# Kernel tuning notes

Measured on AMD Instinct MI355X. Metric: run time of the kernel, lower is better.

## Reference

```python
import jax, jax.numpy as jnp
import numpy as np

L = 16
IN0 = 7  # 3 + 3 + 1 per the torch module
CH = [16, 32, 16]
N = 500000
NEG_SLOPE = 0.2


def setup_inputs() -> dict:
    key = jax.random.key(0)
    ks = jax.random.split(key, 5)
    x = jax.random.normal(ks[0], (N, IN0), dtype=jnp.float32)
    idx = jax.random.randint(ks[1], (N,), 0, L, dtype=jnp.int32)
    # kaiming-uniform-like init scale per layer fan-in
    def init_w(k, shape):
        fan_in = shape[1]
        bound = float(np.sqrt(6.0 / fan_in))
        return jax.random.uniform(k, shape, dtype=jnp.float32, minval=-bound, maxval=bound)
    W0 = init_w(ks[2], (L, IN0, CH[0]))
    W1 = init_w(ks[3], (L, CH[0], CH[1]))
    W2 = init_w(ks[4], (L, CH[1], CH[2]))
    b0 = jnp.zeros((L, CH[0]), dtype=jnp.float32)
    b1 = jnp.zeros((L, CH[1]), dtype=jnp.float32)
    b2 = jnp.zeros((L, CH[2]), dtype=jnp.float32)
    return {"x": x, "idx": idx, "W0": W0, "b0": b0, "W1": W1, "b1": b1, "W2": W2, "b2": b2}


def reference(x, idx, W0, b0, W1, b1, W2, b2):
    # Per-point expert-indexed MLP: h <- LeakyReLU(h @ W[idx] + b[idx]) per layer.
    h = x
    for W, b in ((W0, b0), (W1, b1), (W2, b2)):
        # gather per-point weight [N, in, out] and bias [N, out], vec-mat per point
        h = jax.nn.leaky_relu(
            jnp.einsum("nc,nco->no", h, W[idx]) + b[idx],
            negative_slope=NEG_SLOPE,
        )
    return h
```

## Files before the change

kernel.cpp:

```cpp
#include <hip/hip_runtime.h>
#include <hip/hip_fp16.h>


#define L_EXP 16
#define IN0   7
#define C0    16
#define C1    32
#define C2    16
#define NEG   0.2f
#define BLK   256
#define MPT   4
#define SEGPAD (BLK * MPT)
#define CHUNK  1024
#define NBM    512

#define NW0T 2048
#define NW1T 8192
#define NW2T 8192
#define NWT_TOT (NW0T + NW1T + NW2T)
#define PREPBLK (NWT_TOT / BLK)

#define WS_PART  64
#define WB_W0T   33792
#define WB_W1T   37888
#define WB_W2T   54272
#define WS_PERM  18432

typedef _Float16 h2 __attribute__((ext_vector_type(2)));
union F4H { float4 f4; h2 h[4]; };

__device__ __forceinline__ h2 pk(float a, float b) {
    return __builtin_bit_cast(h2, __builtin_amdgcn_cvt_pkrtz(a, b));
}

__global__ void k_hist(const int* __restrict__ idx, int n, int nblk,
                       int* __restrict__ ws,
                       const float* __restrict__ W0,
                       const float* __restrict__ W1,
                       const float* __restrict__ W2) {
    int t = threadIdx.x;
    if (blockIdx.x >= nblk) {
        int k = (blockIdx.x - nblk) * BLK + t;
        __half* hW0 = (__half*)((char*)ws + WB_W0T);
        __half* hW1 = (__half*)((char*)ws + WB_W1T);
        __half* hW2 = (__half*)((char*)ws + WB_W2T);
        if (k < NW0T) {
            int e = k >> 7, r = k & 127, o = r >> 3, c = r & 7;
            float v = (c < IN0) ? W0[e * (IN0 * C0) + c * C0 + o] : 0.0f;
            hW0[k] = __float2half(v);
        } else if (k < NW0T + NW1T) {
            int k2 = k - NW0T;
            int e = k2 >> 9, r = k2 & 511, o = r >> 4, c = r & 15;
            hW1[k2] = __float2half(W1[e * (C0 * C1) + c * C1 + o]);
        } else {
            int k2 = k - NW0T - NW1T;
            int e = k2 >> 9, r = k2 & 511, o = r >> 5, c = r & 31;
            hW2[k2] = __float2half(W2[e * (C1 * C2) + c * C2 + o]);
        }
        return;
    }
    __shared__ int bins[L_EXP];
    if (t < L_EXP) bins[t] = 0;
    __syncthreads();
    int i4 = blockIdx.x * CHUNK + t * 4;
    if (i4 + 3 < n) {
        int4 v = *reinterpret_cast<const int4*>(idx + i4);
        atomicAdd(&bins[v.x & 15], 1);
        atomicAdd(&bins[v.y & 15], 1);
        atomicAdd(&bins[v.z & 15], 1);
        atomicAdd(&bins[v.w & 15], 1);
    } else {
#pragma unroll
        for (int q = 0; q < 4; ++q)
            if (i4 + q < n) atomicAdd(&bins[idx[i4 + q] & 15], 1);
    }
    __syncthreads();
    if (t < L_EXP) ws[WS_PART + t * NBM + blockIdx.x] = bins[t];
}

__global__ void k_scan(int* __restrict__ ws, int nblk) {
    int t = threadIdx.x;
    int e = t >> 6, l = t & 63;
    int running = 0;
    for (int c = 0; c < nblk; c += 64) {
        int b = c + l;
        int v = (b < nblk) ? ws[WS_PART + e * NBM + b] : 0;
        int s = v;
#pragma unroll
        for (int d = 1; d < 64; d <<= 1) {
            int u = __shfl_up(s, d, 64);
            if (l >= d) s += u;
        }
        if (b < nblk) ws[WS_PART + e * NBM + b] = running + (s - v);
        running += __shfl(s, 63, 64);
    }
    if (l == 0) ws[e] = running;
    __syncthreads();
    if (t == 0) {
        int run = 0;
        for (int q = 0; q < L_EXP; ++q) {
            ws[16 + q] = run;
            run += ((ws[q] + SEGPAD - 1) / SEGPAD) * SEGPAD;
        }
        ws[32] = run;
    }
}

__global__ void k_scatter(const int* __restrict__ idx, int n,
                          int* __restrict__ ws) {
    __shared__ int soff[L_EXP];
    __shared__ int lcount[L_EXP];
    int t = threadIdx.x;
    if (t < L_EXP) {
        soff[t] = ws[16 + t] + ws[WS_PART + t * NBM + blockIdx.x];
        lcount[t] = 0;
    }
    __syncthreads();
    int i4 = blockIdx.x * CHUNK + t * 4;
#pragma unroll
    for (int q = 0; q < 4; ++q) {
        int i = i4 + q;
        if (i < n) {
            int e = idx[i] & 15;
            int r = atomicAdd(&lcount[e], 1);
            ws[WS_PERM + soff[e] + r] = i;
        }
    }
}

__device__ __forceinline__ float leaky(float a) { return fmaxf(a, NEG * a); }

__device__ __forceinline__ float fdot2(h2 a, h2 b, float c) {
    return __builtin_amdgcn_fdot2(a, b, c, false);
}

__global__ void __launch_bounds__(BLK, 2) k_mlp(
    const int* __restrict__ meta, const float* __restrict__ x,
    const float* __restrict__ b0, const float* __restrict__ b1,
    const float* __restrict__ b2, float* __restrict__ out) {
    __shared__ __align__(16) __half sW0t[C0 * 8];
    __shared__ __align__(16) __half sW1t[C1 * C0];
    __shared__ __align__(16) __half sW2t[C2 * C1];
    __shared__ __align__(16) float sB0[C0];
    __shared__ __align__(16) float sB1[C1];
    __shared__ __align__(16) float sB2[C2];

    int start = blockIdx.x * SEGPAD;
    if (start >= meta[32]) return;

    int e = 0;
    while (start >= meta[16 + e + 1]) ++e;
    e = __builtin_amdgcn_readfirstlane(e);

    int t = threadIdx.x;
    {
        const int* w0i = (const int*)((const char*)meta + WB_W0T) + e * 64;
        const int* w1i = (const int*)((const char*)meta + WB_W1T) + e * 256;
        const int* w2i = (const int*)((const char*)meta + WB_W2T) + e * 256;
        if (t < 64) reinterpret_cast<int*>(sW0t)[t] = w0i[t];
        reinterpret_cast<int*>(sW1t)[t] = w1i[t];
        reinterpret_cast<int*>(sW2t)[t] = w2i[t];
        if (t >= 128 && t < 128 + C0) sB0[t - 128] = b0[e * C0 + (t - 128)];
        if (t >= 160 && t < 160 + C1) sB1[t - 160] = b1[e * C1 + (t - 160)];
        if (t >= 192 && t < 192 + C2) sB2[t - 192] = b2[e * C2 + (t - 192)];
    }
    __syncthreads();

    int seg = meta[16 + e];
    int cnt = meta[e];
    int j0 = start - seg + t;

    h2  xh[MPT][4];
    int pid[MPT];
    bool act[MPT];
#pragma unroll
    for (int m = 0; m < MPT; ++m) {
        int j = j0 + m * BLK;
        act[m] = (j < cnt);
        int p = meta[WS_PERM + seg + j];
        pid[m] = act[m] ? p : 0;
        const float* xp = x + (size_t)pid[m] * IN0;
        float4 a = *reinterpret_cast<const float4*>(xp);
        float4 b = *reinterpret_cast<const float4*>(xp + 3);
        xh[m][0] = pk(a.x, a.y);
        xh[m][1] = pk(a.z, a.w);
        xh[m][2] = pk(b.y, b.z);
        xh[m][3] = pk(b.w, 0.0f);
    }
    __builtin_amdgcn_sched_barrier(0);

    float h0f[MPT][C0];
#pragma unroll
    for (int o = 0; o < C0; ++o) {
        F4H u;
        u.f4 = *reinterpret_cast<const float4*>(&sW0t[o * 8]);
#pragma unroll
        for (int m = 0; m < MPT; ++m) {
            float a = sB0[o];
            a = fdot2(xh[m][0], u.h[0], a);
            a = fdot2(xh[m][1], u.h[1], a);
            a = fdot2(xh[m][2], u.h[2], a);
            a = fdot2(xh[m][3], u.h[3], a);
            h0f[m][o] = leaky(a);
        }
        if (o == 7) __builtin_amdgcn_sched_barrier(0);
    }
    h2 h0h[MPT][8];
#pragma unroll
    for (int m = 0; m < MPT; ++m)
#pragma unroll
        for (int p = 0; p < 8; ++p)
            h0h[m][p] = pk(h0f[m][2 * p], h0f[m][2 * p + 1]);
    __builtin_amdgcn_sched_barrier(0);

    float h2a[MPT][C2];
#pragma unroll
    for (int m = 0; m < MPT; ++m)
#pragma unroll
        for (int o = 0; o < C2; ++o) h2a[m][o] = sB2[o];
#pragma unroll 1
    for (int ch = 0; ch < C1 / 8; ++ch) {
        float tvf[MPT][8];
#pragma unroll
        for (int o8 = 0; o8 < 8; ++o8) {
            int o = ch * 8 + o8;
            F4H ua, ub;
            ua.f4 = reinterpret_cast<const float4*>(&sW1t[o * C0])[0];
            ub.f4 = reinterpret_cast<const float4*>(&sW1t[o * C0])[1];
#pragma unroll
            for (int m = 0; m < MPT; ++m) {
                float a = sB1[o];
                a = fdot2(h0h[m][0], ua.h[0], a);
                a = fdot2(h0h[m][1], ua.h[1], a);
                a = fdot2(h0h[m][2], ua.h[2], a);
                a = fdot2(h0h[m][3], ua.h[3], a);
                a = fdot2(h0h[m][4], ub.h[0], a);
                a = fdot2(h0h[m][5], ub.h[1], a);
                a = fdot2(h0h[m][6], ub.h[2], a);
                a = fdot2(h0h[m][7], ub.h[3], a);
                tvf[m][o8] = leaky(a);
            }
        }
        __builtin_amdgcn_sched_barrier(0);
        h2 tvh[MPT][4];
#pragma unroll
        for (int m = 0; m < MPT; ++m)
#pragma unroll
            for (int p = 0; p < 4; ++p)
                tvh[m][p] = pk(tvf[m][2 * p], tvf[m][2 * p + 1]);
#pragma unroll
        for (int o = 0; o < C2; ++o) {
            F4H u;
            u.f4 = *reinterpret_cast<const float4*>(&sW2t[o * C1 + ch * 8]);
#pragma unroll
            for (int m = 0; m < MPT; ++m) {
                float a = h2a[m][o];
                a = fdot2(tvh[m][0], u.h[0], a);
                a = fdot2(tvh[m][1], u.h[1], a);
                a = fdot2(tvh[m][2], u.h[2], a);
                a = fdot2(tvh[m][3], u.h[3], a);
                h2a[m][o] = a;
            }
        }
        __builtin_amdgcn_sched_barrier(0);
    }

#pragma unroll
    for (int m = 0; m < MPT; ++m) {
        if (act[m]) {
            float4* outp = reinterpret_cast<float4*>(out + (size_t)pid[m] * C2);
#pragma unroll
            for (int og = 0; og < C2 / 4; ++og) {
                float4 o;
                o.x = leaky(h2a[m][og * 4 + 0]);
                o.y = leaky(h2a[m][og * 4 + 1]);
                o.z = leaky(h2a[m][og * 4 + 2]);
                o.w = leaky(h2a[m][og * 4 + 3]);
                outp[og] = o;
            }
        }
    }
}

extern "C" void kernel_launch(void* const* d_in, const int* in_sizes, int n_in,
                              void* d_out, int out_size, void* d_ws, size_t ws_size,
                              hipStream_t stream) {
    const float* x  = (const float*)d_in[0];
    const int*  idx = (const int*)d_in[1];
    const float* W0 = (const float*)d_in[2];
    const float* b0 = (const float*)d_in[3];
    const float* W1 = (const float*)d_in[4];
    const float* b1 = (const float*)d_in[5];
    const float* W2 = (const float*)d_in[6];
    const float* b2 = (const float*)d_in[7];
    float* out = (float*)d_out;

    int n = in_sizes[1];
    int* ws = (int*)d_ws;

    int nblk = (n + CHUNK - 1) / CHUNK;
    k_hist<<<nblk + PREPBLK, BLK, 0, stream>>>(idx, n, nblk, ws, W0, W1, W2);
    k_scan<<<1, 1024, 0, stream>>>(ws, nblk);
    k_scatter<<<nblk, BLK, 0, stream>>>(idx, n, ws);

    int mblk = (n + L_EXP * (SEGPAD - 1) + SEGPAD - 1) / SEGPAD;
    k_mlp<<<mblk, BLK, 0, stream>>>(ws, x, b0, b1, b2, out);
}
```

Before: 116.2 us.

## Replace sort-by-expert pipeline with single fused kernel using all-expert LDS weights

Drops the histogram, scan and scatter kernels that grouped points by expert. A single kernel now loads every expert's weights into shared memory as fp16, interleaved by expert so each thread indexes its own expert's slice, and processes points in their original order with coalesced output writes. This removes three launches and the permutation traffic. In exchange, every block pays a 16-expert weight staging cost, and per-thread LDS reads at expert-dependent addresses may cause bank conflicts. Fewer points per thread (two) also lowers register pressure so occupancy can rise.

```diff
diff --git a/kernel.cpp b/kernel.cpp
--- a/kernel.cpp
+++ b/kernel.cpp
@@ -9,22 +9,7 @@
 #define C2    16
 #define NEG   0.2f
 #define BLK   256
-#define MPT   4
-#define SEGPAD (BLK * MPT)
-#define CHUNK  1024
-#define NBM    512
-
-#define NW0T 2048
-#define NW1T 8192
-#define NW2T 8192
-#define NWT_TOT (NW0T + NW1T + NW2T)
-#define PREPBLK (NWT_TOT / BLK)
-
-#define WS_PART  64
-#define WB_W0T   33792
-#define WB_W1T   37888
-#define WB_W2T   54272
-#define WS_PERM  18432
+#define MPT   2
 
 typedef _Float16 h2 __attribute__((ext_vector_type(2)));
 union F4H { float4 f4; h2 h[4]; };
@@ -32,252 +17,153 @@
 __device__ __forceinline__ h2 pk(float a, float b) {
     return __builtin_bit_cast(h2, __builtin_amdgcn_cvt_pkrtz(a, b));
 }
-
-__global__ void k_hist(const int* __restrict__ idx, int n, int nblk,
-                       int* __restrict__ ws,
-                       const float* __restrict__ W0,
-                       const float* __restrict__ W1,
-                       const float* __restrict__ W2) {
-    int t = threadIdx.x;
-    if (blockIdx.x >= nblk) {
-        int k = (blockIdx.x - nblk) * BLK + t;
-        __half* hW0 = (__half*)((char*)ws + WB_W0T);
-        __half* hW1 = (__half*)((char*)ws + WB_W1T);
-        __half* hW2 = (__half*)((char*)ws + WB_W2T);
-        if (k < NW0T) {
-            int e = k >> 7, r = k & 127, o = r >> 3, c = r & 7;
-            float v = (c < IN0) ? W0[e * (IN0 * C0) + c * C0 + o] : 0.0f;
-            hW0[k] = __float2half(v);
-        } else if (k < NW0T + NW1T) {
-            int k2 = k - NW0T;
-            int e = k2 >> 9, r = k2 & 511, o = r >> 4, c = r & 15;
-            hW1[k2] = __float2half(W1[e * (C0 * C1) + c * C1 + o]);
-        } else {
-            int k2 = k - NW0T - NW1T;
-            int e = k2 >> 9, r = k2 & 511, o = r >> 5, c = r & 31;
-            hW2[k2] = __float2half(W2[e * (C1 * C2) + c * C2 + o]);
-        }
-        return;
-    }
-    __shared__ int bins[L_EXP];
-    if (t < L_EXP) bins[t] = 0;
-    __syncthreads();
-    int i4 = blockIdx.x * CHUNK + t * 4;
-    if (i4 + 3 < n) {
-        int4 v = *reinterpret_cast<const int4*>(idx + i4);
-        atomicAdd(&bins[v.x & 15], 1);
-        atomicAdd(&bins[v.y & 15], 1);
-        atomicAdd(&bins[v.z & 15], 1);
-        atomicAdd(&bins[v.w & 15], 1);
-    } else {
-#pragma unroll
-        for (int q = 0; q < 4; ++q)
-            if (i4 + q < n) atomicAdd(&bins[idx[i4 + q] & 15], 1);
-    }
-    __syncthreads();
-    if (t < L_EXP) ws[WS_PART + t * NBM + blockIdx.x] = bins[t];
-}
-
-__global__ void k_scan(int* __restrict__ ws, int nblk) {
-    int t = threadIdx.x;
-    int e = t >> 6, l = t & 63;
-    int running = 0;
-    for (int c = 0; c < nblk; c += 64) {
-        int b = c + l;
-        int v = (b < nblk) ? ws[WS_PART + e * NBM + b] : 0;
-        int s = v;
-#pragma unroll
-        for (int d = 1; d < 64; d <<= 1) {
-            int u = __shfl_up(s, d, 64);
-            if (l >= d) s += u;
-        }
-        if (b < nblk) ws[WS_PART + e * NBM + b] = running + (s - v);
-        running += __shfl(s, 63, 64);
-    }
-    if (l == 0) ws[e] = running;
-    __syncthreads();
-    if (t == 0) {
-        int run = 0;
-        for (int q = 0; q < L_EXP; ++q) {
-            ws[16 + q] = run;
-            run += ((ws[q] + SEGPAD - 1) / SEGPAD) * SEGPAD;
-        }
-        ws[32] = run;
-    }
-}
-
-__global__ void k_scatter(const int* __restrict__ idx, int n,
-                          int* __restrict__ ws) {
-    __shared__ int soff[L_EXP];
-    __shared__ int lcount[L_EXP];
-    int t = threadIdx.x;
-    if (t < L_EXP) {
-        soff[t] = ws[16 + t] + ws[WS_PART + t * NBM + blockIdx.x];
-        lcount[t] = 0;
-    }
-    __syncthreads();
-    int i4 = blockIdx.x * CHUNK + t * 4;
-#pragma unroll
-    for (int q = 0; q < 4; ++q) {
-        int i = i4 + q;
-        if (i < n) {
-            int e = idx[i] & 15;
-            int r = atomicAdd(&lcount[e], 1);
-            ws[WS_PERM + soff[e] + r] = i;
-        }
-    }
-}
-
 __device__ __forceinline__ float leaky(float a) { return fmaxf(a, NEG * a); }
-
 __device__ __forceinline__ float fdot2(h2 a, h2 b, float c) {
     return __builtin_amdgcn_fdot2(a, b, c, false);
 }
 
-__global__ void __launch_bounds__(BLK, 2) k_mlp(
-    const int* __restrict__ meta, const float* __restrict__ x,
-    const float* __restrict__ b0, const float* __restrict__ b1,
-    const float* __restrict__ b2, float* __restrict__ out) {
-    __shared__ __align__(16) __half sW0t[C0 * 8];
-    __shared__ __align__(16) __half sW1t[C1 * C0];
-    __shared__ __align__(16) __half sW2t[C2 * C1];
-    __shared__ __align__(16) float sB0[C0];
-    __shared__ __align__(16) float sB1[C1];
-    __shared__ __align__(16) float sB2[C2];
-
-    int start = blockIdx.x * SEGPAD;
-    if (start >= meta[32]) return;
-
-    int e = 0;
-    while (start >= meta[16 + e + 1]) ++e;
-    e = __builtin_amdgcn_readfirstlane(e);
+__global__ void __launch_bounds__(BLK, 4) k_fused(
+    const float* __restrict__ x, const int* __restrict__ idx,
+    const float* __restrict__ W0, const float* __restrict__ b0,
+    const float* __restrict__ W1, const float* __restrict__ b1,
+    const float* __restrict__ W2, const float* __restrict__ b2,
+    float* __restrict__ out, int n) {
+    __shared__ __align__(16) __half sW0[C0 * L_EXP * 8];
+    __shared__ __align__(16) __half sW1[C1 * 2 * L_EXP * 8];
+    __shared__ __align__(16) __half sW2[C2 * 4 * L_EXP * 8];
+    __shared__ float sB1[C1 * L_EXP];
+    __shared__ float sB2[C2 * L_EXP];
 
     int t = threadIdx.x;
+
     {
-        const int* w0i = (const int*)((const char*)meta + WB_W0T) + e * 64;
-        const int* w1i = (const int*)((const char*)meta + WB_W1T) + e * 256;
-        const int* w2i = (const int*)((const char*)meta + WB_W2T) + e * 256;
-        if (t < 64) reinterpret_cast<int*>(sW0t)[t] = w0i[t];
-        reinterpret_cast<int*>(sW1t)[t] = w1i[t];
-        reinterpret_cast<int*>(sW2t)[t] = w2i[t];
-        if (t >= 128 && t < 128 + C0) sB0[t - 128] = b0[e * C0 + (t - 128)];
-        if (t >= 160 && t < 160 + C1) sB1[t - 160] = b1[e * C1 + (t - 160)];
-        if (t >= 192 && t < 192 + C2) sB2[t - 192] = b2[e * C2 + (t - 192)];
+        int o = t >> 4, e = t & 15;
+        float v0 = W0[e * (IN0 * C0) + 0 * C0 + o];
+        float v1 = W0[e * (IN0 * C0) + 1 * C0 + o];
+        float v2 = W0[e * (IN0 * C0) + 2 * C0 + o];
+        float v3 = W0[e * (IN0 * C0) + 3 * C0 + o];
+        float v4 = W0[e * (IN0 * C0) + 4 * C0 + o];
+        float v5 = W0[e * (IN0 * C0) + 5 * C0 + o];
+        float v6 = W0[e * (IN0 * C0) + 6 * C0 + o];
+        float v7 = b0[e * C0 + o];
+        F4H u;
+        u.h[0] = pk(v0, v1); u.h[1] = pk(v2, v3);
+        u.h[2] = pk(v4, v5); u.h[3] = pk(v6, v7);
+        reinterpret_cast<float4*>(sW0)[t] = u.f4;
+    }
+#pragma unroll
+    for (int rr = 0; rr < 4; ++rr) {
+        int r = rr * BLK + t;
+        int o = r >> 5, q = (r >> 4) & 1, e = r & 15;
+        const float* wp = W1 + e * (C0 * C1) + (q * 8) * C1 + o;
+        F4H u;
+#pragma unroll
+        for (int j = 0; j < 4; ++j)
+            u.h[j] = pk(wp[(2 * j) * C1], wp[(2 * j + 1) * C1]);
+        reinterpret_cast<float4*>(sW1)[r] = u.f4;
+    }
+#pragma unroll
+    for (int rr = 0; rr < 4; ++rr) {
+        int r = rr * BLK + t;
+        int o = r >> 6, q = (r >> 4) & 3, e = r & 15;
+        const float* wp = W2 + e * (C1 * C2) + (q * 8) * C2 + o;
+        F4H u;
+#pragma unroll
+        for (int j = 0; j < 4; ++j)
+            u.h[j] = pk(wp[(2 * j) * C2], wp[(2 * j + 1) * C2]);
+        reinterpret_cast<float4*>(sW2)[r] = u.f4;
+    }
+    {
+        int o = t >> 4, e = t & 15;
+        sB1[t] = b1[e * C1 + o];
+        int r2 = t + 256; int o2 = r2 >> 4, e2 = r2 & 15;
+        sB1[r2] = b1[e2 * C1 + o2];
+        sB2[t] = b2[e * C2 + o];
     }
     __syncthreads();
 
-    int seg = meta[16 + e];
-    int cnt = meta[e];
-    int j0 = start - seg + t;
+    int base = blockIdx.x * (BLK * MPT);
+#pragma unroll 1
+    for (int m = 0; m < MPT; ++m) {
+        int i = base + m * BLK + t;
+        bool act = (i < n);
+        int ii = act ? i : (n - 1);
+        int e = idx[ii] & 15;
 
-    h2  xh[MPT][4];
-    int pid[MPT];
-    bool act[MPT];
+        const float* xp = x + (size_t)ii * IN0;
+        float x0 = xp[0], x1 = xp[1], x2 = xp[2], x3 = xp[3];
+        float x4 = xp[4], x5 = xp[5], x6 = xp[6];
+        h2 xh0 = pk(x0, x1), xh1 = pk(x2, x3);
+        h2 xh2 = pk(x4, x5), xh3 = pk(x6, 1.0f);
+
+        const char* w0p = (const char*)sW0 + e * 16;
+        const char* w1p = (const char*)sW1 + e * 16;
+        const char* w2p = (const char*)sW2 + e * 16;
+
+        h2 h0h[8];
 #pragma unroll
-    for (int m = 0; m < MPT; ++m) {
-        int j = j0 + m * BLK;
-        act[m] = (j < cnt);
-        int p = meta[WS_PERM + seg + j];
-        pid[m] = act[m] ? p : 0;
-        const float* xp = x + (size_t)pid[m] * IN0;
-        float4 a = *reinterpret_cast<const float4*>(xp);
-        float4 b = *reinterpret_cast<const float4*>(xp + 3);
-        xh[m][0] = pk(a.x, a.y);
-        xh[m][1] = pk(a.z, a.w);
-        xh[m][2] = pk(b.y, b.z);
-        xh[m][3] = pk(b.w, 0.0f);
-    }
-    __builtin_amdgcn_sched_barrier(0);
+        for (int op = 0; op < 8; ++op) {
+            F4H ua, ub;
+            ua.f4 = *reinterpret_cast<const float4*>(w0p + (2 * op) * 256);
+            ub.f4 = *reinterpret_cast<const float4*>(w0p + (2 * op + 1) * 256);
+            float a0 = 0.f, a1 = 0.f;
+            a0 = fdot2(xh0, ua.h[0], a0); a1 = fdot2(xh0, ub.h[0], a1);
+            a0 = fdot2(xh1, ua.h[1], a0); a1 = fdot2(xh1, ub.h[1], a1);
+            a0 = fdot2(xh2, ua.h[2], a0); a1 = fdot2(xh2, ub.h[2], a1);
+            a0 = fdot2(xh3, ua.h[3], a0); a1 = fdot2(xh3, ub.h[3], a1);
+            h0h[op] = pk(leaky(a0), leaky(a1));
+        }
 
-    float h0f[MPT][C0];
+        h2 tvh[16];
 #pragma unroll
-    for (int o = 0; o < C0; ++o) {
-        F4H u;
-        u.f4 = *reinterpret_cast<const float4*>(&sW0t[o * 8]);
+        for (int op = 0; op < 16; ++op) {
+            F4H ua, ub, uc, ud;
+            ua.f4 = *reinterpret_cast<const float4*>(w1p + (4 * op + 0) * 256);
+            ub.f4 = *reinterpret_cast<const float4*>(w1p + (4 * op + 1) * 256);
+            uc.f4 = *reinterpret_cast<const float4*>(w1p + (4 * op + 2) * 256);
+            ud.f4 = *reinterpret_cast<const float4*>(w1p + (4 * op + 3) * 256);
+            float a0 = sB1[(2 * op) * 16 + e];
+            float a1 = sB1[(2 * op + 1) * 16 + e];
 #pragma unroll
-        for (int m = 0; m < MPT; ++m) {
-            float a = sB0[o];
-            a = fdot2(xh[m][0], u.h[0], a);
-            a = fdot2(xh[m][1], u.h[1], a);
-            a = fdot2(xh[m][2], u.h[2], a);
-            a = fdot2(xh[m][3], u.h[3], a);
-            h0f[m][o] = leaky(a);
+            for (int p = 0; p < 4; ++p) {
+                a0 = fdot2(h0h[p], ua.h[p], a0);
+                a1 = fdot2(h0h[p], uc.h[p], a1);
+            }
+#pragma unroll
+            for (int p = 0; p < 4; ++p) {
+                a0 = fdot2(h0h[4 + p], ub.h[p], a0);
+                a1 = fdot2(h0h[4 + p], ud.h[p], a1);
+            }
+            tvh[op] = pk(leaky(a0), leaky(a1));
         }
-        if (o == 7) __builtin_amdgcn_sched_barrier(0);
-    }
-    h2 h0h[MPT][8];
-#pragma unroll
-    for (int m = 0; m < MPT; ++m)
-#pragma unroll
-        for (int p = 0; p < 8; ++p)
-            h0h[m][p] = pk(h0f[m][2 * p], h0f[m][2 * p + 1]);
-    __builtin_amdgcn_sched_barrier(0);
 
-    float h2a[MPT][C2];
-#pragma unroll
-    for (int m = 0; m < MPT; ++m)
-#pragma unroll
-        for (int o = 0; o < C2; ++o) h2a[m][o] = sB2[o];
-#pragma unroll 1
-    for (int ch = 0; ch < C1 / 8; ++ch) {
-        float tvf[MPT][8];
-#pragma unroll
-        for (int o8 = 0; o8 < 8; ++o8) {
-            int o = ch * 8 + o8;
-            F4H ua, ub;
-            ua.f4 = reinterpret_cast<const float4*>(&sW1t[o * C0])[0];
-            ub.f4 = reinterpret_cast<const float4*>(&sW1t[o * C0])[1];
-#pragma unroll
-            for (int m = 0; m < MPT; ++m) {
-                float a = sB1[o];
-                a = fdot2(h0h[m][0], ua.h[0], a);
-                a = fdot2(h0h[m][1], ua.h[1], a);
-                a = fdot2(h0h[m][2], ua.h[2], a);
-                a = fdot2(h0h[m][3], ua.h[3], a);
-                a = fdot2(h0h[m][4], ub.h[0], a);
-                a = fdot2(h0h[m][5], ub.h[1], a);
-                a = fdot2(h0h[m][6], ub.h[2], a);
-                a = fdot2(h0h[m][7], ub.h[3], a);
-                tvf[m][o8] = leaky(a);
-            }
-        }
-        __builtin_amdgcn_sched_barrier(0);
-        h2 tvh[MPT][4];
-#pragma unroll
-        for (int m = 0; m < MPT; ++m)
-#pragma unroll
-            for (int p = 0; p < 4; ++p)
-                tvh[m][p] = pk(tvf[m][2 * p], tvf[m][2 * p + 1]);
+        float4 ov[4];
 #pragma unroll
         for (int o = 0; o < C2; ++o) {
-            F4H u;
-            u.f4 = *reinterpret_cast<const float4*>(&sW2t[o * C1 + ch * 8]);
+            F4H ua, ub, uc, ud;
+            ua.f4 = *reinterpret_cast<const float4*>(w2p + (4 * o + 0) * 256);
+            ub.f4 = *reinterpret_cast<const float4*>(w2p + (4 * o + 1) * 256);
+            uc.f4 = *reinterpret_cast<const float4*>(w2p + (4 * o + 2) * 256);
+            ud.f4 = *reinterpret_cast<const float4*>(w2p + (4 * o + 3) * 256);
+            float a = sB2[o * 16 + e];
 #pragma unroll
-            for (int m = 0; m < MPT; ++m) {
-                float a = h2a[m][o];
-                a = fdot2(tvh[m][0], u.h[0], a);
-                a = fdot2(tvh[m][1], u.h[1], a);
-                a = fdot2(tvh[m][2], u.h[2], a);
-                a = fdot2(tvh[m][3], u.h[3], a);
-                h2a[m][o] = a;
-            }
+            for (int p = 0; p < 4; ++p) a = fdot2(tvh[p],      ua.h[p], a);
+#pragma unroll
+            for (int p = 0; p < 4; ++p) a = fdot2(tvh[4 + p],  ub.h[p], a);
+#pragma unroll
+            for (int p = 0; p < 4; ++p) a = fdot2(tvh[8 + p],  uc.h[p], a);
+#pragma unroll
+            for (int p = 0; p < 4; ++p) a = fdot2(tvh[12 + p], ud.h[p], a);
+            float r = leaky(a);
+            if ((o & 3) == 0) ov[o >> 2].x = r;
+            else if ((o & 3) == 1) ov[o >> 2].y = r;
+            else if ((o & 3) == 2) ov[o >> 2].z = r;
+            else ov[o >> 2].w = r;
         }
-        __builtin_amdgcn_sched_barrier(0);
-    }
 
-#pragma unroll
-    for (int m = 0; m < MPT; ++m) {
-        if (act[m]) {
-            float4* outp = reinterpret_cast<float4*>(out + (size_t)pid[m] * C2);
-#pragma unroll
-            for (int og = 0; og < C2 / 4; ++og) {
-                float4 o;
-                o.x = leaky(h2a[m][og * 4 + 0]);
-                o.y = leaky(h2a[m][og * 4 + 1]);
-                o.z = leaky(h2a[m][og * 4 + 2]);
-                o.w = leaky(h2a[m][og * 4 + 3]);
-                outp[og] = o;
-            }
+        if (act) {
+            float4* op = reinterpret_cast<float4*>(out + (size_t)i * C2);
+            op[0] = ov[0]; op[1] = ov[1]; op[2] = ov[2]; op[3] = ov[3];
         }
     }
 }
@@ -296,13 +182,6 @@
     float* out = (float*)d_out;
 
     int n = in_sizes[1];
-    int* ws = (int*)d_ws;
-
-    int nblk = (n + CHUNK - 1) / CHUNK;
-    k_hist<<<nblk + PREPBLK, BLK, 0, stream>>>(idx, n, nblk, ws, W0, W1, W2);
-    k_scan<<<1, 1024, 0, stream>>>(ws, nblk);
-    k_scatter<<<nblk, BLK, 0, stream>>>(idx, n, ws);
-
-    int mblk = (n + L_EXP * (SEGPAD - 1) + SEGPAD - 1) / SEGPAD;
-    k_mlp<<<mblk, BLK, 0, stream>>>(ws, x, b0, b1, b2, out);
+    int blocks = (n + BLK * MPT - 1) / (BLK * MPT);
+    k_fused<<<blocks, BLK, 0, stream>>>(x, idx, W0, b0, W1, b1, W2, b2, out, n);
 }
```

Result: slower. 127.8 us (+10.0%).
